# Kernel optimization log

Hardware: AMD Instinct MI355X
Metric: run time of the kernel (lower is better)

Reference implementation:

```python
import jax, jax.numpy as jnp
import numpy as np
from jax import lax

SIZES = [(159, 159), (159, 159), (79, 79), (79, 79), (39, 39), (19, 19), (19, 19), (19, 19)]
STRIDES = [4, 4, 8, 8, 16, 32, 32, 32]
RF_SIZES = [55.0, 71.0, 111.0, 143.0, 223.0, 383.0, 511.0, 639.0]
SCORE_THR = 0.35
IOU_THR = 0.5
MAX_BOXES = 100
BATCH = 32
CLS_C = 3  # class_num + 1


def _coords_fmap2orig(size, stride):
    h, w = size
    ys = (jnp.arange(h, dtype=jnp.float32) * stride + stride / 2.0)
    xs = (jnp.arange(w, dtype=jnp.float32) * stride + stride / 2.0)
    X, Y = jnp.meshgrid(xs, ys)  # row-major over (h, w)
    return jnp.stack([X.reshape(-1), Y.reshape(-1)], axis=-1)  # [h*w, 2]


def _flatten_cat(branches):
    # each branch [b,c,h,w] -> [b,h*w,c]; concat over anchors
    outs = [x.transpose(0, 2, 3, 1).reshape(x.shape[0], -1, x.shape[1]) for x in branches]
    return jnp.concatenate(outs, axis=1)


def _nms_keep(boxes, valid):
    # boxes [K,4] sorted by score desc, valid [K] bool. Greedy NMS, +1 area convention.
    x1, y1, x2, y2 = boxes[:, 0], boxes[:, 1], boxes[:, 2], boxes[:, 3]
    areas = (x2 - x1 + 1.0) * (y2 - y1 + 1.0)
    xmin = jnp.maximum(x1[:, None], x1[None, :])
    ymin = jnp.maximum(y1[:, None], y1[None, :])
    xmax = jnp.minimum(x2[:, None], x2[None, :])
    ymax = jnp.minimum(y2[:, None], y2[None, :])
    inter = jnp.clip(xmax - xmin, 0.0) * jnp.clip(ymax - ymin, 0.0)
    iou = inter / (areas[:, None] + areas[None, :] - inter)
    idx = jnp.arange(boxes.shape[0])

    def body(i, keep):
        sup = (iou[i] > IOU_THR) & (idx > i) & keep[i]
        return keep & ~sup

    return lax.fori_loop(0, boxes.shape[0], body, valid)


def setup_inputs() -> dict:
    key = jax.random.key(0)
    inp = {}
    ks = jax.random.split(key, 16)
    for i, (h, w) in enumerate(SIZES):
        inp[f"cls{i}"] = jax.random.normal(ks[i], (BATCH, CLS_C, h, w), dtype=jnp.float32)
        inp[f"reg{i}"] = jax.random.normal(ks[8 + i], (BATCH, 4, h, w), dtype=jnp.float32)
    return inp


def reference(cls0, cls1, cls2, cls3, cls4, cls5, cls6, cls7,
              reg0, reg1, reg2, reg3, reg4, reg5, reg6, reg7):
    cls_branches = [cls0, cls1, cls2, cls3, cls4, cls5, cls6, cls7]
    reg_branches = [reg0, reg1, reg2, reg3, reg4, reg5, reg6, reg7]

    cls_logits = _flatten_cat(cls_branches)   # [B, N, 3]
    reg_preds = _flatten_cat(reg_branches)    # [B, N, 4]
    coords = jnp.concatenate([_coords_fmap2orig(s, st) for s, st in zip(SIZES, STRIDES)], axis=0)  # [N,2]

    cls_preds = jax.nn.softmax(cls_logits, axis=2)
    cls_scores = jnp.max(cls_preds, axis=2)      # [B,N]
    cls_classes = jnp.argmax(cls_preds, axis=2)  # [B,N]

    rf_scale = jnp.concatenate([
        jnp.full((h * w,), rf / 2.0, dtype=jnp.float32) for (h, w), rf in zip(SIZES, RF_SIZES)
    ])  # [N]
    reg_preds = reg_preds * rf_scale[None, :, None]
    x1y1 = coords[None, :, :] - reg_preds[..., :2]
    x2y2 = coords[None, :, :] + reg_preds[..., 2:]
    boxes = jnp.concatenate([x1y1, x2y2], axis=2)  # [B,N,4]

    # foreground mask -> mask scores so topk picks fg first
    fg = cls_classes > 0
    masked_scores = jnp.where(fg, cls_scores, -1.0)
    top_scores, top_idx = lax.top_k(masked_scores, MAX_BOXES)  # [B,K], sorted desc
    top_boxes = jnp.take_along_axis(boxes, top_idx[..., None], axis=1)      # [B,K,4]
    top_classes = jnp.take_along_axis(cls_classes, top_idx, axis=1)         # [B,K]

    valid = (top_scores >= SCORE_THR) & (top_classes > 0)
    keep = jax.vmap(_nms_keep)(top_boxes, valid)  # [B,K] bool

    out_scores = jnp.where(keep, top_scores, 0.0)
    out_classes = jnp.where(keep, top_classes, 0)
    out_boxes = jnp.where(keep[..., None], top_boxes, 0.0)
    return out_scores, out_classes, out_boxes, keep
```

## Files before the change

### kernel.cpp

```cpp
#include <hip/hip_runtime.h>
#include <stdint.h>

#define N_ANCH 65648
#define NQ16   (N_ANCH / 16)
#define NCHUNK 65
#define CHUNK  1024
#define CAP    4096
#define KBASE  0xBE800000u
#define NBATCH 32
#define TOPK   100
#define FT     1024

struct Ptrs { const float* cls[8]; const float* reg[8]; };

__constant__ int   c_off[9] = {0,25281,50562,56803,63044,64565,64926,65287,65648};
__constant__ int   c_sz[8]  = {159,159,79,79,39,19,19,19};
__constant__ float c_st[8]  = {4.f,4.f,8.f,8.f,16.f,32.f,32.f,32.f};
__constant__ float c_rf[8]  = {27.5f,35.5f,55.5f,71.5f,111.5f,191.5f,255.5f,319.5f};

__device__ inline uint32_t anchor_key(const Ptrs& p, int b, int n) {
  int k = 0;
#pragma unroll
  for (int q = 1; q < 8; ++q) if (n >= c_off[q]) k = q;
  int local = n - c_off[k];
  int hw = c_sz[k] * c_sz[k];
  const float* c = p.cls[k] + (size_t)(b * 3) * hw + local;
  float l0 = c[0], l1 = c[(size_t)hw], l2 = c[(size_t)2 * hw];
  float m = l0; int cl = 0;
  if (l1 > m) { m = l1; cl = 1; }
  if (l2 > m) { m = l2; cl = 2; }
  if (cl == 0) return 0u;
  float s = 1.0f / (expf(l0 - m) + expf(l1 - m) + expf(l2 - m));
  return __float_as_uint(s) | 0x80000000u;
}

__global__ __launch_bounds__(256) void k_bins(Ptrs p, uint8_t* bins, uint16_t* hist) {
  int bid = blockIdx.x;
  int b = bid / NCHUNK, chunk = bid % NCHUNK;
  int t = threadIdx.x;
  __shared__ uint32_t lh[256];
  lh[t] = 0;
  __syncthreads();
  int n0 = chunk * CHUNK + t * 4;
  if (n0 < N_ANCH) {
    uchar4 v; uint8_t* vb = (uint8_t*)&v;
#pragma unroll
    for (int u = 0; u < 4; ++u) {
      uint32_t key = anchor_key(p, b, n0 + u);
      uint8_t bin = key ? (uint8_t)((key - KBASE) >> 16) : (uint8_t)0;
      vb[u] = bin;
      if (bin) atomicAdd(&lh[bin], 1u);
    }
    *(uchar4*)(bins + (size_t)b * N_ANCH + n0) = v;
  }
  __syncthreads();
  hist[((size_t)b * NCHUNK + chunk) * 256 + t] = (uint16_t)lh[t];
}

template<int U>
__device__ inline void rank_select(const unsigned long long* s_all, int c, int c8, int t,
                                   unsigned long long* top) {
  unsigned long long mine[U]; int rk[U];
#pragma unroll
  for (int u = 0; u < U; ++u) {
    int i = t + u * FT;
    mine[u] = (i < c) ? s_all[i] : 0ull;
    rk[u] = 0;
  }
  for (int j = 0; j < c8; j += 8) {
    unsigned long long v0 = s_all[j+0], v1 = s_all[j+1], v2 = s_all[j+2], v3 = s_all[j+3];
    unsigned long long v4 = s_all[j+4], v5 = s_all[j+5], v6 = s_all[j+6], v7 = s_all[j+7];
#pragma unroll
    for (int u = 0; u < U; ++u) {
      rk[u] += (v0 > mine[u]) + (v1 > mine[u]) + (v2 > mine[u]) + (v3 > mine[u])
             + (v4 > mine[u]) + (v5 > mine[u]) + (v6 > mine[u]) + (v7 > mine[u]);
    }
  }
#pragma unroll
  for (int u = 0; u < U; ++u) {
    int i = t + u * FT;
    if (i < c && rk[u] < TOPK) top[rk[u]] = mine[u];
  }
}

__global__ __launch_bounds__(FT) void k_sel(Ptrs p, const uint8_t* bins,
                                            const uint16_t* hist, float* out) {
  int b = blockIdx.x, t = threadIdx.x;
  __shared__ uint32_t part[4][256];
  __shared__ uint32_t tot[256];
  __shared__ int s_idx[CAP];
  __shared__ unsigned long long s_all[CAP + 8];
  __shared__ unsigned long long top[TOPK];
  __shared__ float bx1[TOPK], by1[TOPK], bx2[TOPK], by2[TOPK], area[TOPK], sc[TOPK];
  __shared__ int cls_s[TOPK], keep[TOPK];
  __shared__ uint32_t s_cnt;
  __shared__ int s_thr;

  {
    const uint16_t* hb = hist + (size_t)b * NCHUNK * 256;
    int g = t >> 8, tb = t & 255;
    uint32_t v = 0;
    for (int ch = g; ch < NCHUNK; ch += 4) v += hb[ch * 256 + tb];
    part[g][tb] = v;
    if (t == 0) s_cnt = 0;
    if (t < TOPK) top[t] = 0ull;
    __syncthreads();
    if (t < 256) tot[t] = part[0][t] + part[1][t] + part[2][t] + part[3][t];
    __syncthreads();
    for (int d = 1; d < 256; d <<= 1) {
      uint32_t add = 0;
      if (t < 256 && t + d < 256) add = tot[t + d];
      __syncthreads();
      if (t < 256) tot[t] += add;
      __syncthreads();
    }
    if (t < 256) {
      uint32_t suf = tot[t], sufn = (t < 255) ? tot[t + 1] : 0u;
      if (suf >= TOPK && sufn < TOPK) s_thr = t;
      if (t == 0 && tot[0] < TOPK) s_thr = 0;
    }
    __syncthreads();
  }
  int thr = s_thr; if (thr < 1) thr = 1;

  {
    const uint4* bp = (const uint4*)(bins + (size_t)b * N_ANCH);
    for (int i = t; i < NQ16; i += FT) {
      uint4 v4 = bp[i];
      uint32_t ws[4] = { v4.x, v4.y, v4.z, v4.w };
#pragma unroll
      for (int w = 0; w < 4; ++w) {
        uint32_t wv = ws[w];
        if (!wv) continue;
#pragma unroll
        for (int u = 0; u < 4; ++u) {
          int bin = (wv >> (8 * u)) & 0xFF;
          if (bin >= thr) {
            uint32_t q = atomicAdd(&s_cnt, 1u);
            if (q < CAP) s_idx[q] = i * 16 + w * 4 + u;
          }
        }
      }
    }
  }
  __syncthreads();
  int c = (int)min(s_cnt, (uint32_t)CAP);
  int c8 = (c + 7) & ~7;

  for (int i = t; i < c; i += FT) {
    int n = s_idx[i];
    uint32_t key = anchor_key(p, b, n);
    s_all[i] = ((unsigned long long)key << 32) | (uint32_t)(~(uint32_t)n);
  }
  for (int i = c + t; i < c8; i += FT) s_all[i] = 0ull;
  __syncthreads();

  if      (c <= FT)     rank_select<1>(s_all, c, c8, t, top);
  else if (c <= 2 * FT) rank_select<2>(s_all, c, c8, t, top);
  else                  rank_select<4>(s_all, c, c8, t, top);
  __syncthreads();

  int r = t;
  if (r < TOPK) {
    unsigned long long pk = top[r];
    if (pk == 0ull) {
      sc[r] = -1.f; cls_s[r] = 0; keep[r] = 0;
      bx1[r] = by1[r] = bx2[r] = by2[r] = 0.f; area[r] = 1.f;
    } else {
      uint32_t key = (uint32_t)(pk >> 32);
      int n = (int)(~(uint32_t)pk);
      float score = __uint_as_float(key & 0x7FFFFFFFu);
      int k2 = 0;
#pragma unroll
      for (int q = 1; q < 8; ++q) if (n >= c_off[q]) k2 = q;
      int local = n - c_off[k2];
      int w = c_sz[k2], hw = w * w;
      int i2 = local / w, j2 = local % w;
      const float* cp = p.cls[k2] + (size_t)(b * 3) * hw + local;
      float l0 = cp[0], l1 = cp[(size_t)hw], l2 = cp[(size_t)2 * hw];
      float m = l0; int cl = 0;
      if (l1 > m) { m = l1; cl = 1; }
      if (l2 > m) { m = l2; cl = 2; }
      const float* rp = p.reg[k2] + (size_t)(b * 4) * hw + local;
      float r0 = rp[0], r1 = rp[(size_t)hw], r2 = rp[(size_t)2 * hw], r3 = rp[(size_t)3 * hw];
      float st = c_st[k2], rf = c_rf[k2];
      float cx = (float)j2 * st + st * 0.5f;
      float cy = (float)i2 * st + st * 0.5f;
      float x1 = cx - r0 * rf, y1 = cy - r1 * rf;
      float x2 = cx + r2 * rf, y2 = cy + r3 * rf;
      sc[r] = score; cls_s[r] = cl;
      bx1[r] = x1; by1[r] = y1; bx2[r] = x2; by2[r] = y2;
      area[r] = (x2 - x1 + 1.0f) * (y2 - y1 + 1.0f);
      keep[r] = (score >= 0.35f && cl > 0) ? 1 : 0;
    }
  }
  __syncthreads();

  if (t < 64) {
    int r0 = t, r1 = t + 64;
    float a1x = bx1[r0], a1y = by1[r0], a2x = bx2[r0], a2y = by2[r0], aA = area[r0];
    int k0 = keep[r0];
    bool has1 = (r1 < TOPK);
    float c1x = 0.f, c1y = 0.f, c2x = 0.f, c2y = 0.f, cA = 1.f;
    int k1 = 0;
    if (has1) { c1x = bx1[r1]; c1y = by1[r1]; c2x = bx2[r1]; c2y = by2[r1]; cA = area[r1]; k1 = keep[r1]; }
    for (int i = 0; i < TOPK; ++i) {
      int ol = i & 63, sl = i >> 6;
      int   ki  = __shfl(sl ? k1  : k0,  ol);
      float ix1 = __shfl(sl ? c1x : a1x, ol);
      float iy1 = __shfl(sl ? c1y : a1y, ol);
      float ix2 = __shfl(sl ? c2x : a2x, ol);
      float iy2 = __shfl(sl ? c2y : a2y, ol);
      float iA  = __shfl(sl ? cA  : aA,  ol);
      if (ki) {
        if (k0 && r0 > i) {
          float xmin = fmaxf(ix1, a1x), ymin = fmaxf(iy1, a1y);
          float xmax = fminf(ix2, a2x), ymax = fminf(iy2, a2y);
          float inter = fmaxf(xmax - xmin, 0.f) * fmaxf(ymax - ymin, 0.f);
          float iou = inter / (iA + aA - inter);
          if (iou > 0.5f) k0 = 0;
        }
        if (has1 && k1 && r1 > i) {
          float xmin = fmaxf(ix1, c1x), ymin = fmaxf(iy1, c1y);
          float xmax = fminf(ix2, c2x), ymax = fminf(iy2, c2y);
          float inter = fmaxf(xmax - xmin, 0.f) * fmaxf(ymax - ymin, 0.f);
          float iou = inter / (iA + cA - inter);
          if (iou > 0.5f) k1 = 0;
        }
      }
    }
    keep[r0] = k0;
    if (has1) keep[r1] = k1;
  }
  __syncthreads();

  if (r < TOPK) {
    int o = b * TOPK + r;
    bool kp = keep[r] != 0;
    out[o] = kp ? sc[r] : 0.f;
    out[NBATCH * TOPK + o] = kp ? (float)cls_s[r] : 0.f;
    float* ob = out + 2 * NBATCH * TOPK + (size_t)o * 4;
    ob[0] = kp ? bx1[r] : 0.f;
    ob[1] = kp ? by1[r] : 0.f;
    ob[2] = kp ? bx2[r] : 0.f;
    ob[3] = kp ? by2[r] : 0.f;
    out[6 * NBATCH * TOPK + o] = kp ? 1.f : 0.f;
  }
}

extern "C" void kernel_launch(void* const* d_in, const int* in_sizes, int n_in,
                              void* d_out, int out_size, void* d_ws, size_t ws_size,
                              hipStream_t stream) {
  Ptrs p;
  for (int i = 0; i < 8; ++i) {
    p.cls[i] = (const float*)d_in[2 * i];
    p.reg[i] = (const float*)d_in[2 * i + 1];
  }
  uint8_t*  bins = (uint8_t*)d_ws;
  uint16_t* hist = (uint16_t*)((char*)d_ws + 2100736);
  float* out = (float*)d_out;

  k_bins<<<NBATCH * NCHUNK, 256, 0, stream>>>(p, bins, hist);
  k_sel<<<NBATCH, FT, 0, stream>>>(p, bins, hist, out);
}
```

Measured before the change: 57.56 us.

## Split selection into multi-block compaction kernel plus single-wave rank/NMS kernel

```diff
diff --git a/kernel.cpp b/kernel.cpp
--- a/kernel.cpp
+++ b/kernel.cpp
@@ -2,14 +2,15 @@
 #include <stdint.h>
 
 #define N_ANCH 65648
-#define NQ16   (N_ANCH / 16)
 #define NCHUNK 65
 #define CHUNK  1024
-#define CAP    4096
+#define NQ16   4103
+#define NSLICE 8
+#define SEGCAP 1024
+#define CAP    1024
 #define KBASE  0xBE800000u
 #define NBATCH 32
 #define TOPK   100
-#define FT     1024
 
 struct Ptrs { const float* cls[8]; const float* reg[8]; };
 
@@ -57,13 +58,77 @@
   hist[((size_t)b * NCHUNK + chunk) * 256 + t] = (uint16_t)lh[t];
 }
 
+__global__ __launch_bounds__(256) void k_mid(Ptrs p, const uint8_t* bins,
+                                             const uint16_t* hist,
+                                             unsigned long long* seg, uint32_t* cnt) {
+  int bid = blockIdx.x;
+  int b = bid / NSLICE, sl = bid % NSLICE;
+  int t = threadIdx.x;
+  __shared__ uint32_t tot[256];
+  __shared__ int s_thr;
+  __shared__ uint32_t s_cnt;
+
+  const uint16_t* hb = hist + (size_t)b * NCHUNK * 256;
+  uint32_t v0 = 0, v1 = 0, v2 = 0, v3 = 0;
+  int ch = 0;
+  for (; ch + 4 <= NCHUNK; ch += 4) {
+    v0 += hb[(ch + 0) * 256 + t];
+    v1 += hb[(ch + 1) * 256 + t];
+    v2 += hb[(ch + 2) * 256 + t];
+    v3 += hb[(ch + 3) * 256 + t];
+  }
+  for (; ch < NCHUNK; ++ch) v0 += hb[ch * 256 + t];
+  tot[t] = v0 + v1 + v2 + v3;
+  if (t == 0) s_cnt = 0;
+  __syncthreads();
+  for (int d = 1; d < 256; d <<= 1) {
+    uint32_t add = (t + d < 256) ? tot[t + d] : 0u;
+    __syncthreads();
+    tot[t] += add;
+    __syncthreads();
+  }
+  uint32_t suf = tot[t], sufn = (t < 255) ? tot[t + 1] : 0u;
+  if (suf >= TOPK && sufn < TOPK) s_thr = t;
+  if (t == 0 && tot[0] < TOPK) s_thr = 0;
+  __syncthreads();
+  int thr = s_thr; if (thr < 1) thr = 1;
+
+  int ch0 = sl * 9, ch1 = min(ch0 + 9, NCHUNK);
+  int q0 = ch0 * 64, q1 = min(ch1 * 64, NQ16);
+  const uint4* bp = (const uint4*)(bins + (size_t)b * N_ANCH);
+  unsigned long long* sg = seg + (size_t)bid * SEGCAP;
+  for (int i = q0 + t; i < q1; i += 256) {
+    uint4 v4 = bp[i];
+    uint32_t ws[4] = { v4.x, v4.y, v4.z, v4.w };
+#pragma unroll
+    for (int w = 0; w < 4; ++w) {
+      uint32_t wv = ws[w];
+      if (!wv) continue;
+#pragma unroll
+      for (int u = 0; u < 4; ++u) {
+        int bin = (wv >> (8 * u)) & 0xFF;
+        if (bin >= thr) {
+          uint32_t pos = atomicAdd(&s_cnt, 1u);
+          if (pos < SEGCAP) {
+            int n = i * 16 + w * 4 + u;
+            uint32_t key = anchor_key(p, b, n);
+            sg[pos] = ((unsigned long long)key << 32) | (uint32_t)(~(uint32_t)n);
+          }
+        }
+      }
+    }
+  }
+  __syncthreads();
+  if (t == 0) cnt[bid] = s_cnt;
+}
+
 template<int U>
-__device__ inline void rank_select(const unsigned long long* s_all, int c, int c8, int t,
-                                   unsigned long long* top) {
+__device__ inline void rank_sel64(const unsigned long long* s_all, int c, int c8, int t,
+                                  unsigned long long* top) {
   unsigned long long mine[U]; int rk[U];
 #pragma unroll
   for (int u = 0; u < U; ++u) {
-    int i = t + u * FT;
+    int i = t + u * 64;
     mine[u] = (i < c) ? s_all[i] : 0ull;
     rk[u] = 0;
   }
@@ -78,90 +143,48 @@
   }
 #pragma unroll
   for (int u = 0; u < U; ++u) {
-    int i = t + u * FT;
+    int i = t + u * 64;
     if (i < c && rk[u] < TOPK) top[rk[u]] = mine[u];
   }
 }
 
-__global__ __launch_bounds__(FT) void k_sel(Ptrs p, const uint8_t* bins,
-                                            const uint16_t* hist, float* out) {
+__global__ __launch_bounds__(64) void k_nms(Ptrs p, const uint32_t* cnt,
+                                            const unsigned long long* seg, float* out) {
   int b = blockIdx.x, t = threadIdx.x;
-  __shared__ uint32_t part[4][256];
-  __shared__ uint32_t tot[256];
-  __shared__ int s_idx[CAP];
   __shared__ unsigned long long s_all[CAP + 8];
   __shared__ unsigned long long top[TOPK];
   __shared__ float bx1[TOPK], by1[TOPK], bx2[TOPK], by2[TOPK], area[TOPK], sc[TOPK];
   __shared__ int cls_s[TOPK], keep[TOPK];
-  __shared__ uint32_t s_cnt;
-  __shared__ int s_thr;
-
-  {
-    const uint16_t* hb = hist + (size_t)b * NCHUNK * 256;
-    int g = t >> 8, tb = t & 255;
-    uint32_t v = 0;
-    for (int ch = g; ch < NCHUNK; ch += 4) v += hb[ch * 256 + tb];
-    part[g][tb] = v;
-    if (t == 0) s_cnt = 0;
-    if (t < TOPK) top[t] = 0ull;
-    __syncthreads();
-    if (t < 256) tot[t] = part[0][t] + part[1][t] + part[2][t] + part[3][t];
-    __syncthreads();
-    for (int d = 1; d < 256; d <<= 1) {
-      uint32_t add = 0;
-      if (t < 256 && t + d < 256) add = tot[t + d];
-      __syncthreads();
-      if (t < 256) tot[t] += add;
-      __syncthreads();
-    }
-    if (t < 256) {
-      uint32_t suf = tot[t], sufn = (t < 255) ? tot[t + 1] : 0u;
-      if (suf >= TOPK && sufn < TOPK) s_thr = t;
-      if (t == 0 && tot[0] < TOPK) s_thr = 0;
-    }
-    __syncthreads();
-  }
-  int thr = s_thr; if (thr < 1) thr = 1;
-
-  {
-    const uint4* bp = (const uint4*)(bins + (size_t)b * N_ANCH);
-    for (int i = t; i < NQ16; i += FT) {
-      uint4 v4 = bp[i];
-      uint32_t ws[4] = { v4.x, v4.y, v4.z, v4.w };
-#pragma unroll
-      for (int w = 0; w < 4; ++w) {
-        uint32_t wv = ws[w];
-        if (!wv) continue;
-#pragma unroll
-        for (int u = 0; u < 4; ++u) {
-          int bin = (wv >> (8 * u)) & 0xFF;
-          if (bin >= thr) {
-            uint32_t q = atomicAdd(&s_cnt, 1u);
-            if (q < CAP) s_idx[q] = i * 16 + w * 4 + u;
-          }
-        }
-      }
-    }
-  }
-  __syncthreads();
-  int c = (int)min(s_cnt, (uint32_t)CAP);
+
+  uint32_t pf[NSLICE + 1];
+  pf[0] = 0;
+#pragma unroll
+  for (int s = 0; s < NSLICE; ++s) {
+    uint32_t cs = cnt[b * NSLICE + s];
+    if (cs > SEGCAP) cs = SEGCAP;
+    pf[s + 1] = pf[s] + cs;
+  }
+  int c = (int)min(pf[NSLICE], (uint32_t)CAP);
   int c8 = (c + 7) & ~7;
 
-  for (int i = t; i < c; i += FT) {
-    int n = s_idx[i];
-    uint32_t key = anchor_key(p, b, n);
-    s_all[i] = ((unsigned long long)key << 32) | (uint32_t)(~(uint32_t)n);
-  }
-  for (int i = c + t; i < c8; i += FT) s_all[i] = 0ull;
-  __syncthreads();
-
-  if      (c <= FT)     rank_select<1>(s_all, c, c8, t, top);
-  else if (c <= 2 * FT) rank_select<2>(s_all, c, c8, t, top);
-  else                  rank_select<4>(s_all, c, c8, t, top);
-  __syncthreads();
-
-  int r = t;
-  if (r < TOPK) {
+  for (int i = t; i < c; i += 64) {
+    int s = 0;
+#pragma unroll
+    for (int q = 1; q < NSLICE; ++q) if (i >= (int)pf[q]) s = q;
+    s_all[i] = seg[((size_t)b * NSLICE + s) * SEGCAP + (i - (int)pf[s])];
+  }
+  for (int i = c + t; i < c8; i += 64) s_all[i] = 0ull;
+  for (int r = t; r < TOPK; r += 64) top[r] = 0ull;
+  __syncthreads();
+
+  if      (c <= 64)  rank_sel64<1>(s_all, c, c8, t, top);
+  else if (c <= 128) rank_sel64<2>(s_all, c, c8, t, top);
+  else if (c <= 256) rank_sel64<4>(s_all, c, c8, t, top);
+  else if (c <= 512) rank_sel64<8>(s_all, c, c8, t, top);
+  else               rank_sel64<16>(s_all, c, c8, t, top);
+  __syncthreads();
+
+  for (int r = t; r < TOPK; r += 64) {
     unsigned long long pk = top[r];
     if (pk == 0ull) {
       sc[r] = -1.f; cls_s[r] = 0; keep[r] = 0;
@@ -196,7 +219,7 @@
   }
   __syncthreads();
 
-  if (t < 64) {
+  {
     int r0 = t, r1 = t + 64;
     float a1x = bx1[r0], a1y = by1[r0], a2x = bx2[r0], a2y = by2[r0], aA = area[r0];
     int k0 = keep[r0];
@@ -234,7 +257,7 @@
   }
   __syncthreads();
 
-  if (r < TOPK) {
+  for (int r = t; r < TOPK; r += 64) {
     int o = b * TOPK + r;
     bool kp = keep[r] != 0;
     out[o] = kp ? sc[r] : 0.f;
@@ -258,8 +281,12 @@
   }
   uint8_t*  bins = (uint8_t*)d_ws;
   uint16_t* hist = (uint16_t*)((char*)d_ws + 2100736);
+  uint32_t* cnt  = (uint32_t*)((char*)d_ws + 3165696);
+  unsigned long long* seg =
+      (unsigned long long*)((char*)d_ws + 3166720);
   float* out = (float*)d_out;
 
   k_bins<<<NBATCH * NCHUNK, 256, 0, stream>>>(p, bins, hist);
-  k_sel<<<NBATCH, FT, 0, stream>>>(p, bins, hist, out);
-}
+  k_mid<<<NBATCH * NSLICE, 256, 0, stream>>>(p, bins, hist, seg, cnt);
+  k_nms<<<NBATCH, 64, 0, stream>>>(p, cnt, seg, out);
+}
```

Measured after the change: 67.29 us. 1.17x slower.

## Replace sequential shuffle NMS with precomputed suppression bitmasks and serial mask sweep

Applied to the files above, without the earlier changes.

```diff
diff --git a/kernel.cpp b/kernel.cpp
--- a/kernel.cpp
+++ b/kernel.cpp
@@ -2,10 +2,10 @@
 #include <stdint.h>
 
 #define N_ANCH 65648
-#define NQ16   (N_ANCH / 16)
 #define NCHUNK 65
 #define CHUNK  1024
-#define CAP    4096
+#define NQ16   4103
+#define CAP    2048
 #define KBASE  0xBE800000u
 #define NBATCH 32
 #define TOPK   100
@@ -93,15 +93,22 @@
   __shared__ unsigned long long top[TOPK];
   __shared__ float bx1[TOPK], by1[TOPK], bx2[TOPK], by2[TOPK], area[TOPK], sc[TOPK];
   __shared__ int cls_s[TOPK], keep[TOPK];
+  __shared__ unsigned long long sup0[TOPK], sup1[TOPK];
+  __shared__ unsigned long long s_km[2], s_km2[2];
   __shared__ uint32_t s_cnt;
   __shared__ int s_thr;
 
   {
     const uint16_t* hb = hist + (size_t)b * NCHUNK * 256;
     int g = t >> 8, tb = t & 255;
-    uint32_t v = 0;
-    for (int ch = g; ch < NCHUNK; ch += 4) v += hb[ch * 256 + tb];
-    part[g][tb] = v;
+    uint32_t v0 = 0, v1 = 0, v2 = 0, v3 = 0;
+    for (int ch = g; ch < NCHUNK; ch += 16) {
+      v0 += hb[ch * 256 + tb];
+      if (ch + 4 < NCHUNK)  v1 += hb[(ch + 4) * 256 + tb];
+      if (ch + 8 < NCHUNK)  v2 += hb[(ch + 8) * 256 + tb];
+      if (ch + 12 < NCHUNK) v3 += hb[(ch + 12) * 256 + tb];
+    }
+    part[g][tb] = v0 + v1 + v2 + v3;
     if (t == 0) s_cnt = 0;
     if (t < TOPK) top[t] = 0ull;
     __syncthreads();
@@ -149,19 +156,17 @@
 
   for (int i = t; i < c; i += FT) {
     int n = s_idx[i];
-    uint32_t key = anchor_key(p, b, n);
-    s_all[i] = ((unsigned long long)key << 32) | (uint32_t)(~(uint32_t)n);
+    s_all[i] = ((unsigned long long)anchor_key(p, b, n) << 32) | (uint32_t)(~(uint32_t)n);
   }
   for (int i = c + t; i < c8; i += FT) s_all[i] = 0ull;
   __syncthreads();
 
-  if      (c <= FT)     rank_select<1>(s_all, c, c8, t, top);
-  else if (c <= 2 * FT) rank_select<2>(s_all, c, c8, t, top);
-  else                  rank_select<4>(s_all, c, c8, t, top);
-  __syncthreads();
-
-  int r = t;
-  if (r < TOPK) {
+  if (c <= FT) rank_select<1>(s_all, c, c8, t, top);
+  else         rank_select<2>(s_all, c, c8, t, top);
+  __syncthreads();
+
+  if (t < TOPK) {
+    int r = t;
     unsigned long long pk = top[r];
     if (pk == 0ull) {
       sc[r] = -1.f; cls_s[r] = 0; keep[r] = 0;
@@ -196,47 +201,53 @@
   }
   __syncthreads();
 
+  if (t < TOPK) {
+    float a1x = bx1[t], a1y = by1[t], a2x = bx2[t], a2y = by2[t], aA = area[t];
+    unsigned long long m0 = 0, m1 = 0;
+    for (int j = t + 1; j < TOPK; ++j) {
+      float xmin = fmaxf(a1x, bx1[j]), ymin = fmaxf(a1y, by1[j]);
+      float xmax = fminf(a2x, bx2[j]), ymax = fminf(a2y, by2[j]);
+      float inter = fmaxf(xmax - xmin, 0.f) * fmaxf(ymax - ymin, 0.f);
+      float iou = inter / (aA + area[j] - inter);
+      if (iou > 0.5f) { if (j < 64) m0 |= 1ull << j; else m1 |= 1ull << (j - 64); }
+    }
+    sup0[t] = m0; sup1[t] = m1;
+  }
   if (t < 64) {
-    int r0 = t, r1 = t + 64;
-    float a1x = bx1[r0], a1y = by1[r0], a2x = bx2[r0], a2y = by2[r0], aA = area[r0];
-    int k0 = keep[r0];
-    bool has1 = (r1 < TOPK);
-    float c1x = 0.f, c1y = 0.f, c2x = 0.f, c2y = 0.f, cA = 1.f;
-    int k1 = 0;
-    if (has1) { c1x = bx1[r1]; c1y = by1[r1]; c2x = bx2[r1]; c2y = by2[r1]; cA = area[r1]; k1 = keep[r1]; }
-    for (int i = 0; i < TOPK; ++i) {
-      int ol = i & 63, sl = i >> 6;
-      int   ki  = __shfl(sl ? k1  : k0,  ol);
-      float ix1 = __shfl(sl ? c1x : a1x, ol);
-      float iy1 = __shfl(sl ? c1y : a1y, ol);
-      float ix2 = __shfl(sl ? c2x : a2x, ol);
-      float iy2 = __shfl(sl ? c2y : a2y, ol);
-      float iA  = __shfl(sl ? cA  : aA,  ol);
-      if (ki) {
-        if (k0 && r0 > i) {
-          float xmin = fmaxf(ix1, a1x), ymin = fmaxf(iy1, a1y);
-          float xmax = fminf(ix2, a2x), ymax = fminf(iy2, a2y);
-          float inter = fmaxf(xmax - xmin, 0.f) * fmaxf(ymax - ymin, 0.f);
-          float iou = inter / (iA + aA - inter);
-          if (iou > 0.5f) k0 = 0;
-        }
-        if (has1 && k1 && r1 > i) {
-          float xmin = fmaxf(ix1, c1x), ymin = fmaxf(iy1, c1y);
-          float xmax = fminf(ix2, c2x), ymax = fminf(iy2, c2y);
-          float inter = fmaxf(xmax - xmin, 0.f) * fmaxf(ymax - ymin, 0.f);
-          float iou = inter / (iA + cA - inter);
-          if (iou > 0.5f) k1 = 0;
+    unsigned long long m = __ballot(keep[t] != 0);
+    if (t == 0) s_km[0] = m;
+  } else if (t < 128) {
+    unsigned long long m = __ballot(t < TOPK && keep[t] != 0);
+    if (t == 64) s_km[1] = m;
+  }
+  __syncthreads();
+
+  if (t == 0) {
+    unsigned long long km0 = s_km[0], km1 = s_km[1];
+    for (int i0 = 0; i0 < TOPK; i0 += 8) {
+      unsigned long long a0[8], a1[8];
+#pragma unroll
+      for (int q = 0; q < 8; ++q) {
+        int i = i0 + q;
+        a0[q] = (i < TOPK) ? sup0[i] : 0ull;
+        a1[q] = (i < TOPK) ? sup1[i] : 0ull;
+      }
+#pragma unroll
+      for (int q = 0; q < 8; ++q) {
+        int i = i0 + q;
+        if (i < TOPK) {
+          bool ki = (i < 64) ? ((km0 >> i) & 1) : ((km1 >> (i - 64)) & 1);
+          if (ki) { km0 &= ~a0[q]; km1 &= ~a1[q]; }
         }
       }
     }
-    keep[r0] = k0;
-    if (has1) keep[r1] = k1;
-  }
-  __syncthreads();
-
-  if (r < TOPK) {
-    int o = b * TOPK + r;
-    bool kp = keep[r] != 0;
+    s_km2[0] = km0; s_km2[1] = km1;
+  }
+  __syncthreads();
+
+  if (t < TOPK) {
+    int r = t, o = b * TOPK + r;
+    bool kp = (r < 64) ? ((s_km2[0] >> r) & 1) : ((s_km2[1] >> (r - 64)) & 1);
     out[o] = kp ? sc[r] : 0.f;
     out[NBATCH * TOPK + o] = kp ? (float)cls_s[r] : 0.f;
     float* ob = out + 2 * NBATCH * TOPK + (size_t)o * 4;
```

Result: faster. 49.16 us (-14.6%).
